# Performance work log

Measured on AMD Instinct MI355X. Metric: run time of the kernel, lower is better.

The kernel has to match this reference:

```python
import jax, jax.numpy as jnp
import numpy as np
import math

ANCHORS = np.array([[[10,13],[16,30],[33,23]],
                    [[30,61],[62,45],[59,119]],
                    [[116,90],[156,198],[373,326]]], dtype=np.float32)
STRIDES = [8.0, 16.0, 32.0]
BALANCE = [4.0, 1.0, 0.4]
LAMBDA_BOX, LAMBDA_OBJ, LAMBDA_CLS = 0.05, 1.0, 0.5
ANCHOR_T = 4.0
CP, CN = 1.0, 0.0  # label_smoothing = 0
EPS = 1e-7


def _bce(x, t):
    # BCEWithLogits, elementwise, numerically stable
    return jnp.maximum(x, 0.) - x * t + jnp.log1p(jnp.exp(-jnp.abs(x)))


def _ciou(b1, b2):
    # b1, b2: (M, 4) xyxy
    ix1 = jnp.maximum(b1[:, 0], b2[:, 0]); iy1 = jnp.maximum(b1[:, 1], b2[:, 1])
    ix2 = jnp.minimum(b1[:, 2], b2[:, 2]); iy2 = jnp.minimum(b1[:, 3], b2[:, 3])
    inter = jnp.clip(ix2 - ix1, 0.) * jnp.clip(iy2 - iy1, 0.)
    a1 = (b1[:, 2] - b1[:, 0]) * (b1[:, 3] - b1[:, 1])
    a2 = (b2[:, 2] - b2[:, 0]) * (b2[:, 3] - b2[:, 1])
    union = a1 + a2 - inter + EPS
    iou = inter / union
    ex1 = jnp.minimum(b1[:, 0], b2[:, 0]); ey1 = jnp.minimum(b1[:, 1], b2[:, 1])
    ex2 = jnp.maximum(b1[:, 2], b2[:, 2]); ey2 = jnp.maximum(b1[:, 3], b2[:, 3])
    c2 = (ex2 - ex1) ** 2 + (ey2 - ey1) ** 2 + EPS
    # center distance^2: centers are (x1+x2)/2
    rho2 = ((b1[:, 0] + b1[:, 2] - b2[:, 0] - b2[:, 2]) ** 2 +
            (b1[:, 1] + b1[:, 3] - b2[:, 1] - b2[:, 3]) ** 2) / 4.
    w1 = b1[:, 2] - b1[:, 0]; h1 = b1[:, 3] - b1[:, 1]
    w2 = b2[:, 2] - b2[:, 0]; h2 = b2[:, 3] - b2[:, 1]
    v = (4. / math.pi ** 2) * (jnp.arctan(w2 / (h2 + EPS)) - jnp.arctan(w1 / (h1 + EPS))) ** 2
    alpha = jax.lax.stop_gradient(v / (1. - iou + v + EPS))  # torch.no_grad()
    return iou - rho2 / c2 - alpha * v


def _layer_loss(pred, targets, anchor, balance):
    # pred: (B, na, H, W, 5+nc); targets: (nt, 6); anchor: (na, 2) in grid units
    B, na, H, W, C = pred.shape
    nc = C - 5
    nt = targets.shape[0]
    gain = jnp.array([1., 1., W, H, W, H], jnp.float32)
    t = targets * gain  # (nt, 6): [b, cls, gx, gy, gw, gh]
    # anchor-ratio filter
    r = t[:, 4:6][None] / (anchor[:, None] + 1e-16)            # (na, nt, 2)
    anchor_ok = jnp.max(jnp.maximum(r, 1. / r), axis=2) < ANCHOR_T  # (na, nt)
    # neighbor-cell selection masks (center + 4 neighbors)
    gxy = t[:, 2:4]
    gxi = jnp.floor(gxy)
    frac = gxy - gxi
    jm = (frac[:, 0] > .5) & (gxi[:, 0] < W - 1)
    km = (frac[:, 1] > .5) & (gxi[:, 1] < H - 1)
    lm = (frac[:, 0] < .5) & (gxi[:, 0] > 0)
    mm = (frac[:, 1] < .5) & (gxi[:, 1] > 0)
    sel = jnp.stack([jnp.ones_like(jm), jm, km, lm, mm])       # (5, nt)
    valid = sel[:, None, :] & anchor_ok[None]                  # (5, na, nt)
    off = jnp.array([[0, 0], [1, 0], [0, 1], [-1, 0], [0, -1]], jnp.float32)
    gxy_e = gxy[None] - off[:, None]                           # (5, nt, 2)
    gi = jnp.clip(jnp.floor(gxy_e).astype(jnp.int32), 0,
                  jnp.array([W - 1, H - 1], jnp.int32))        # (5, nt, 2)
    txy = gxy_e - gi.astype(jnp.float32)                       # offset-form xy
    gwh = t[:, 4:6]
    tbox = jnp.concatenate([txy - gwh[None] / 2., txy + gwh[None] / 2.], -1)  # (5, nt, 4)
    # flatten fixed-size candidate set (5 * na * nt), masked by `valid`
    shp = (5, na, nt)
    b_idx = jnp.broadcast_to(t[:, 0].astype(jnp.int32)[None, None], shp).reshape(-1)
    cls_i = jnp.broadcast_to(t[:, 1].astype(jnp.int32)[None, None], shp).reshape(-1)
    a_idx = jnp.broadcast_to(jnp.arange(na)[None, :, None], shp).reshape(-1)
    gx = jnp.broadcast_to(gi[:, None, :, 0], shp).reshape(-1)
    gy = jnp.broadcast_to(gi[:, None, :, 1], shp).reshape(-1)
    tbox_f = jnp.broadcast_to(tbox[:, None], shp + (4,)).reshape(-1, 4)
    vmask = valid.reshape(-1).astype(pred.dtype)
    cnt = vmask.sum()
    # fancy-indexed gather of matched predictions
    pm = pred[b_idx, a_idx, gy, gx]                            # (M, C)
    pxy = jax.nn.sigmoid(pm[:, :2]) * 2. - 0.5
    pwh = (jax.nn.sigmoid(pm[:, 2:4]) * 2.) ** 2 * anchor[a_idx]
    pbox = jnp.concatenate([pxy - pwh / 2., pxy + pwh / 2.], -1)
    ciou = _ciou(pbox, tbox_f)
    lbox = jnp.where(cnt > 0, jnp.sum((1. - ciou) * vmask) / jnp.maximum(cnt, 1.), 0.)
    # objectness target scatter (detached, clamped CIoU); invalid write 0 -> no-op under max
    tobj = jnp.zeros(pred.shape[:4], pred.dtype)
    vals = jax.lax.stop_gradient(jnp.clip(ciou, 0.) * vmask)
    tobj = tobj.at[b_idx, a_idx, gy, gx].max(vals)
    lobj = jnp.mean(_bce(pred[..., 4], tobj)) * balance
    # classification (mean over matched rows x nc elems)
    ct = CN + (CP - CN) * jax.nn.one_hot(cls_i, nc, dtype=pm.dtype)
    lcls = jnp.where(cnt > 0,
                     jnp.sum(_bce(pm[:, 5:], ct) * vmask[:, None]) / jnp.maximum(cnt * nc, 1.),
                     0.)
    return lbox, lobj, lcls


def _forward(pred0, pred1, pred2, targets):
    B = pred0.shape[0]
    preds = [pred0, pred1, pred2]
    lb = lo = lc = 0.
    for i in range(3):
        anchor = jnp.asarray(ANCHORS[i]) / STRIDES[i]
        bx, ob, cl = _layer_loss(preds[i], targets, anchor, BALANCE[i])
        lb = lb + bx; lo = lo + ob; lc = lc + cl
    return (LAMBDA_BOX * lb + LAMBDA_OBJ * lo + LAMBDA_CLS * lc) * B


def setup_inputs() -> dict:
    key = jax.random.key(0)
    ks = jax.random.split(key, 7)
    B, NT = 16, 300
    pred0 = jax.random.normal(ks[0], (B, 3, 80, 80, 85), jnp.float32)
    pred1 = jax.random.normal(ks[1], (B, 3, 40, 40, 85), jnp.float32)
    pred2 = jax.random.normal(ks[2], (B, 3, 20, 20, 85), jnp.float32)
    b = jax.random.randint(ks[3], (NT, 1), 0, B).astype(jnp.float32)
    c = jax.random.randint(ks[4], (NT, 1), 0, 80).astype(jnp.float32)
    cxy = jax.random.uniform(ks[5], (NT, 2), jnp.float32, 0.02, 0.98)
    wh = jax.random.uniform(ks[6], (NT, 2), jnp.float32, 0.02, 0.3)
    targets = jnp.concatenate([b, c, cxy, wh], axis=1)  # (NT, 6)
    return {"pred0": pred0, "pred1": pred1, "pred2": pred2, "targets": targets}


def reference(pred0, pred1, pred2, targets):
    return _forward(pred0, pred1, pred2, targets)
```

## Files before the change

kernel.cpp:

```cpp
#include <hip/hip_runtime.h>
#include <math.h>

#define EPSF 1e-7f
#define NT 256

__device__ __constant__ float d_anch[3][3][2] = {
    {{10.f/8.f,  13.f/8.f},  {16.f/8.f,  30.f/8.f},  {33.f/8.f,  23.f/8.f}},
    {{30.f/16.f, 61.f/16.f}, {62.f/16.f, 45.f/16.f}, {59.f/16.f, 119.f/16.f}},
    {{116.f/32.f,90.f/32.f}, {156.f/32.f,198.f/32.f},{373.f/32.f,326.f/32.f}},
};

__device__ __forceinline__ float bce0(float x) {
    return fmaxf(x, 0.0f) + log1pf(expf(-fabsf(x)));
}
__device__ __forceinline__ float bcef(float x, float t) {
    return fmaxf(x, 0.0f) - x * t + log1pf(expf(-fabsf(x)));
}
__device__ __forceinline__ float sigm(float x) {
    return 1.0f / (1.0f + expf(-x));
}

__device__ __forceinline__ float wave_reduce(float v) {
    #pragma unroll
    for (int off = 32; off > 0; off >>= 1) v += __shfl_down(v, off, 64);
    return v;
}

__global__ void __launch_bounds__(NT)
stream_kernel(const float* __restrict__ pred0,
              const float* __restrict__ pred1,
              const float* __restrict__ pred2,
              float* __restrict__ tobj,
              float* __restrict__ objpart,
              int n0, int n1, int n2)
{
    int N = n0 + n1 + n2;
    int base = blockIdx.x * (NT * 4) + threadIdx.x;
    float acc = 0.0f;
    #pragma unroll
    for (int k = 0; k < 4; ++k) {
        int idx = base + k * NT;
        if (idx < N) {
            tobj[idx] = 0.0f;
            const float* pred; int cell; float w;
            if (idx < n0)           { pred = pred0; cell = idx;           w = 4.0f / (float)n0; }
            else if (idx < n0 + n1) { pred = pred1; cell = idx - n0;      w = 1.0f / (float)n1; }
            else                    { pred = pred2; cell = idx - n0 - n1; w = 0.4f / (float)n2; }
            acc += w * bce0(pred[(size_t)cell * 85 + 4]);
        }
    }
    __shared__ float s[4];
    float r = wave_reduce(acc);
    if ((threadIdx.x & 63) == 0) s[threadIdx.x >> 6] = r;
    __syncthreads();
    if (threadIdx.x == 0)
        objpart[blockIdx.x] = s[0] + s[1] + s[2] + s[3];
}

__global__ void __launch_bounds__(NT)
entry_kernel(const float* __restrict__ pred0,
             const float* __restrict__ pred1,
             const float* __restrict__ pred2,
             const float* __restrict__ targets,
             int nt, int bpl,
             float* __restrict__ tobj_base,
             float* __restrict__ blockpart,
             int n0, int n1, int n2)
{
    int layer = blockIdx.x / bpl;
    int sub   = blockIdx.x % bpl;
    int wid   = threadIdx.x >> 6;
    int lane  = threadIdx.x & 63;
    int perLayer = 15 * nt;
    int eL = sub * 4 + wid;

    const float* pred; float* tobj; int H, W; float wl;
    if (layer == 0)      { pred = pred0; tobj = tobj_base;           H = 80; W = 80; wl = 4.0f / (float)n0; }
    else if (layer == 1) { pred = pred1; tobj = tobj_base + n0;      H = 40; W = 40; wl = 1.0f / (float)n1; }
    else                 { pred = pred2; tobj = tobj_base + n0 + n1; H = 20; W = 20; wl = 0.4f / (float)n2; }

    float lbox = 0.0f, cnt = 0.0f, corr = 0.0f, clsacc = 0.0f;

    if (eL < perLayer) {
        int t = eL % nt;
        int a = (eL / nt) % 3;
        int o = eL / (nt * 3);

        const float* tg = targets + t * 6;
        float tb = tg[0], tc = tg[1];
        float gx = tg[2] * (float)W, gy = tg[3] * (float)H;
        float gw = tg[4] * (float)W, gh = tg[5] * (float)H;

        float aw = d_anch[layer][a][0], ah = d_anch[layer][a][1];
        float rw = gw / (aw + 1e-16f), rh = gh / (ah + 1e-16f);
        float rmax = fmaxf(fmaxf(rw, 1.0f / rw), fmaxf(rh, 1.0f / rh));
        bool aok = rmax < 4.0f;

        float fxi = floorf(gx), fyi = floorf(gy);
        float fx = gx - fxi, fy = gy - fyi;
        bool selo;
        switch (o) {
            case 0: selo = true; break;
            case 1: selo = (fx > 0.5f) && (fxi < (float)(W - 1)); break;
            case 2: selo = (fy > 0.5f) && (fyi < (float)(H - 1)); break;
            case 3: selo = (fx < 0.5f) && (fxi > 0.0f); break;
            default: selo = (fy < 0.5f) && (fyi > 0.0f); break;
        }

        if (aok && selo) {
            float ox = (o == 1) ? 1.0f : (o == 3) ? -1.0f : 0.0f;
            float oy = (o == 2) ? 1.0f : (o == 4) ? -1.0f : 0.0f;
            float gex = gx - ox, gey = gy - oy;
            int gix = min(max((int)floorf(gex), 0), W - 1);
            int giy = min(max((int)floorf(gey), 0), H - 1);
            float txc = gex - (float)gix, tyc = gey - (float)giy;
            float tx1 = txc - gw * 0.5f, ty1 = tyc - gh * 0.5f;
            float tx2 = txc + gw * 0.5f, ty2 = tyc + gh * 0.5f;

            int b = (int)tb, cls = (int)tc;
            int cell = (int)(((((size_t)b * 3 + a) * H + giy) * W + gix));
            const float* pm = pred + (size_t)cell * 85;

            float p0 = pm[0], p1v = pm[1], p2v = pm[2], p3 = pm[3];
            float pxc = sigm(p0) * 2.0f - 0.5f;
            float pyc = sigm(p1v) * 2.0f - 0.5f;
            float sw = sigm(p2v) * 2.0f;
            float sh = sigm(p3) * 2.0f;
            float pw = sw * sw * aw, ph = sh * sh * ah;
            float px1 = pxc - pw * 0.5f, py1 = pyc - ph * 0.5f;
            float px2 = pxc + pw * 0.5f, py2 = pyc + ph * 0.5f;

            float ix1 = fmaxf(px1, tx1), iy1 = fmaxf(py1, ty1);
            float ix2 = fminf(px2, tx2), iy2 = fminf(py2, ty2);
            float inter = fmaxf(ix2 - ix1, 0.0f) * fmaxf(iy2 - iy1, 0.0f);
            float a1 = (px2 - px1) * (py2 - py1);
            float a2 = (tx2 - tx1) * (ty2 - ty1);
            float uni = a1 + a2 - inter + EPSF;
            float iou = inter / uni;
            float ex1 = fminf(px1, tx1), ey1 = fminf(py1, ty1);
            float ex2 = fmaxf(px2, tx2), ey2 = fmaxf(py2, ty2);
            float cw = ex2 - ex1, chh = ey2 - ey1;
            float c2 = cw * cw + chh * chh + EPSF;
            float dx = px1 + px2 - tx1 - tx2;
            float dy = py1 + py2 - ty1 - ty2;
            float rho2 = (dx * dx + dy * dy) * 0.25f;
            float w1 = px2 - px1, h1 = py2 - py1;
            float w2 = tx2 - tx1, h2 = ty2 - ty1;
            float dat = atanf(w2 / (h2 + EPSF)) - atanf(w1 / (h1 + EPSF));
            float v = 0.40528473f * dat * dat;
            float alpha = v / (1.0f - iou + v + EPSF);
            float ciou = iou - rho2 / c2 - alpha * v;

            if (lane == 0) {
                lbox = 1.0f - ciou;
                cnt = 1.0f;
                float vobj = fmaxf(ciou, 0.0f);
                unsigned int oldb = atomicMax((unsigned int*)&tobj[cell],
                                              __float_as_uint(vobj));
                float old = __uint_as_float(oldb);
                float nw = fmaxf(vobj, old);
                corr = wl * pm[4] * (nw - old);
            }

            float xc = pm[5 + lane];
            clsacc = bcef(xc, (lane == cls) ? 1.0f : 0.0f);
            if (lane < 16) {
                float xc2 = pm[69 + lane];
                clsacc += bcef(xc2, ((64 + lane) == cls) ? 1.0f : 0.0f);
            }
        }
    }

    float rb = wave_reduce(lbox);
    float rc = wave_reduce(cnt);
    float rl = wave_reduce(clsacc);
    float rr = wave_reduce(corr);
    __shared__ float s[4][4];
    if (lane == 0) {
        s[wid][0] = rb; s[wid][1] = rc; s[wid][2] = rl; s[wid][3] = rr;
    }
    __syncthreads();
    if (threadIdx.x < 4) {
        float v = s[0][threadIdx.x] + s[1][threadIdx.x] +
                  s[2][threadIdx.x] + s[3][threadIdx.x];
        blockpart[(size_t)blockIdx.x * 4 + threadIdx.x] = v;
    }
}

__global__ void __launch_bounds__(NT)
final_kernel(const float* __restrict__ objpart, int nb1,
             const float* __restrict__ blockpart, int bpl,
             float* __restrict__ out, int B)
{
    __shared__ float s[4];
    __shared__ float comp[11];
    int tid = threadIdx.x;
    int lane = tid & 63;
    int wid = tid >> 6;

    float v = 0.0f;
    for (int i = tid; i < nb1; i += NT) v += objpart[i];
    v = wave_reduce(v);
    if (lane == 0) s[wid] = v;
    __syncthreads();
    if (tid == 0) comp[9] = s[0] + s[1] + s[2] + s[3];
    __syncthreads();

    for (int c = 0; c < 4; ++c) {
        for (int L = 0; L < 3; ++L) {
            float v2 = 0.0f;
            if (c < 3) {
                for (int i = tid; i < bpl; i += NT)
                    v2 += blockpart[(size_t)(L * bpl + i) * 4 + c];
            } else if (L == 0) {
                for (int i = tid; i < 3 * bpl; i += NT)
                    v2 += blockpart[(size_t)i * 4 + 3];
            } else continue;
            v2 = wave_reduce(v2);
            if (lane == 0) s[wid] = v2;
            __syncthreads();
            if (tid == 0) {
                float r = s[0] + s[1] + s[2] + s[3];
                if (c < 3) comp[L * 3 + c] = r; else comp[10] = r;
            }
            __syncthreads();
        }
    }

    if (tid == 0) {
        float lobj = comp[9] - comp[10];
        float lb = 0.0f, lc = 0.0f;
        for (int L = 0; L < 3; ++L) {
            float cb = comp[L * 3 + 0], cc = comp[L * 3 + 1], cl = comp[L * 3 + 2];
            if (cc > 0.0f) {
                lb += cb / fmaxf(cc, 1.0f);
                lc += cl / fmaxf(cc * 80.0f, 1.0f);
            }
        }
        out[0] = (0.05f * lb + lobj + 0.5f * lc) * (float)B;
    }
}

extern "C" void kernel_launch(void* const* d_in, const int* in_sizes, int n_in,
                              void* d_out, int out_size, void* d_ws, size_t ws_size,
                              hipStream_t stream) {
    const float* pred0 = (const float*)d_in[0];
    const float* pred1 = (const float*)d_in[1];
    const float* pred2 = (const float*)d_in[2];
    const float* targets = (const float*)d_in[3];

    int B = in_sizes[0] / (3 * 80 * 80 * 85);
    int nt = in_sizes[3] / 6;
    int n0 = B * 3 * 80 * 80;
    int n1 = B * 3 * 40 * 40;
    int n2 = B * 3 * 20 * 20;
    int N = n0 + n1 + n2;
    int NB1 = (N + NT * 4 - 1) / (NT * 4);
    int perLayer = 15 * nt;
    int bpl = (perLayer + 3) / 4;
    int grid2 = 3 * bpl;

    float* tobj = (float*)d_ws;
    float* objpart = tobj + N;
    float* blockpart = objpart + NB1;

    stream_kernel<<<NB1, NT, 0, stream>>>(
        pred0, pred1, pred2, tobj, objpart, n0, n1, n2);
    entry_kernel<<<grid2, NT, 0, stream>>>(
        pred0, pred1, pred2, targets, nt, bpl, tobj, blockpart, n0, n1, n2);
    final_kernel<<<1, NT, 0, stream>>>(
        objpart, NB1, blockpart, bpl, (float*)d_out, B);
}
```

Before: 41.41 us.

## Replace strided objectness gather with coalesced float4 sweep fused into target kernel

The objectness BCE pass no longer loads one float per 85-float cell. Instead a fixed set of blocks streams the whole prediction tensors as coalesced float4 loads and keeps only the lanes that hold channel 4. These sweep blocks are merged into the same launch as the per-target box/class kernel, and zeroing of tobj moves to its own small vectorized kernel. The aim is fully coalesced memory traffic and overlap of the two phases, at the cost of reading every byte of the predictions rather than only the cache lines that contain objectness values.

New measurement: 64.88 us. +56.7%, slower.

```diff
diff --git a/kernel.cpp b/kernel.cpp
--- a/kernel.cpp
+++ b/kernel.cpp
@@ -3,6 +3,8 @@
 
 #define EPSF 1e-7f
 #define NT 256
+#define SWEEP_BLOCKS 1536
+#define ZERO_BLOCKS 512
 
 __device__ __constant__ float d_anch[3][3][2] = {
     {{10.f/8.f,  13.f/8.f},  {16.f/8.f,  30.f/8.f},  {33.f/8.f,  23.f/8.f}},
@@ -19,7 +21,6 @@
 __device__ __forceinline__ float sigm(float x) {
     return 1.0f / (1.0f + expf(-x));
 }
-
 __device__ __forceinline__ float wave_reduce(float v) {
     #pragma unroll
     for (int off = 32; off > 0; off >>= 1) v += __shfl_down(v, off, 64);
@@ -27,57 +28,65 @@
 }
 
 __global__ void __launch_bounds__(NT)
-stream_kernel(const float* __restrict__ pred0,
-              const float* __restrict__ pred1,
-              const float* __restrict__ pred2,
-              float* __restrict__ tobj,
-              float* __restrict__ objpart,
-              int n0, int n1, int n2)
+zero_kernel(float4* __restrict__ p, int n4)
 {
-    int N = n0 + n1 + n2;
-    int base = blockIdx.x * (NT * 4) + threadIdx.x;
-    float acc = 0.0f;
-    #pragma unroll
-    for (int k = 0; k < 4; ++k) {
-        int idx = base + k * NT;
-        if (idx < N) {
-            tobj[idx] = 0.0f;
-            const float* pred; int cell; float w;
-            if (idx < n0)           { pred = pred0; cell = idx;           w = 4.0f / (float)n0; }
-            else if (idx < n0 + n1) { pred = pred1; cell = idx - n0;      w = 1.0f / (float)n1; }
-            else                    { pred = pred2; cell = idx - n0 - n1; w = 0.4f / (float)n2; }
-            acc += w * bce0(pred[(size_t)cell * 85 + 4]);
-        }
-    }
-    __shared__ float s[4];
-    float r = wave_reduce(acc);
-    if ((threadIdx.x & 63) == 0) s[threadIdx.x >> 6] = r;
-    __syncthreads();
-    if (threadIdx.x == 0)
-        objpart[blockIdx.x] = s[0] + s[1] + s[2] + s[3];
+    for (int i = blockIdx.x * NT + threadIdx.x; i < n4; i += ZERO_BLOCKS * NT)
+        p[i] = make_float4(0.f, 0.f, 0.f, 0.f);
 }
 
 __global__ void __launch_bounds__(NT)
-entry_kernel(const float* __restrict__ pred0,
-             const float* __restrict__ pred1,
-             const float* __restrict__ pred2,
-             const float* __restrict__ targets,
-             int nt, int bpl,
-             float* __restrict__ tobj_base,
-             float* __restrict__ blockpart,
-             int n0, int n1, int n2)
+work_kernel(const float* __restrict__ pred0,
+            const float* __restrict__ pred1,
+            const float* __restrict__ pred2,
+            const float* __restrict__ targets,
+            int nt, int bpl,
+            float* __restrict__ tobj_base,
+            float* __restrict__ objpart,
+            float* __restrict__ blockpart,
+            int n0, int n1, int n2)
 {
-    int layer = blockIdx.x / bpl;
-    int sub   = blockIdx.x % bpl;
+    float w0 = 4.0f / (float)n0, w1 = 1.0f / (float)n1, w2 = 0.4f / (float)n2;
+
+    if (blockIdx.x < SWEEP_BLOCKS) {
+        unsigned f40 = (unsigned)n0 / 4u * 85u;
+        unsigned f41 = (unsigned)n1 / 4u * 85u;
+        unsigned f42 = (unsigned)n2 / 4u * 85u;
+        unsigned totalF4 = f40 + f41 + f42;
+        float acc = 0.0f;
+        for (unsigned f = blockIdx.x * NT + threadIdx.x; f < totalF4;
+             f += SWEEP_BLOCKS * NT) {
+            const float4* src; unsigned l; float w;
+            if (f < f40)              { src = (const float4*)pred0; l = f;              w = w0; }
+            else if (f < f40 + f41)   { src = (const float4*)pred1; l = f - f40;        w = w1; }
+            else                      { src = (const float4*)pred2; l = f - f40 - f41;  w = w2; }
+            float4 q = src[l];
+            unsigned m = (4u * l) % 85u;
+            if (m >= 1u && m <= 4u) {
+                float v = (m == 4u) ? q.x : (m == 3u) ? q.y : (m == 2u) ? q.z : q.w;
+                acc += w * bce0(v);
+            }
+        }
+        __shared__ float s[4];
+        float r = wave_reduce(acc);
+        if ((threadIdx.x & 63) == 0) s[threadIdx.x >> 6] = r;
+        __syncthreads();
+        if (threadIdx.x == 0)
+            objpart[blockIdx.x] = s[0] + s[1] + s[2] + s[3];
+        return;
+    }
+
+    int eb    = blockIdx.x - SWEEP_BLOCKS;
+    int layer = eb / bpl;
+    int sub   = eb % bpl;
     int wid   = threadIdx.x >> 6;
     int lane  = threadIdx.x & 63;
     int perLayer = 15 * nt;
     int eL = sub * 4 + wid;
 
     const float* pred; float* tobj; int H, W; float wl;
-    if (layer == 0)      { pred = pred0; tobj = tobj_base;           H = 80; W = 80; wl = 4.0f / (float)n0; }
-    else if (layer == 1) { pred = pred1; tobj = tobj_base + n0;      H = 40; W = 40; wl = 1.0f / (float)n1; }
-    else                 { pred = pred2; tobj = tobj_base + n0 + n1; H = 20; W = 20; wl = 0.4f / (float)n2; }
+    if (layer == 0)      { pred = pred0; tobj = tobj_base;           H = 80; W = 80; wl = w0; }
+    else if (layer == 1) { pred = pred1; tobj = tobj_base + n0;      H = 40; W = 40; wl = w1; }
+    else                 { pred = pred2; tobj = tobj_base + n0 + n1; H = 20; W = 20; wl = w2; }
 
     float lbox = 0.0f, cnt = 0.0f, corr = 0.0f, clsacc = 0.0f;
 
@@ -144,9 +153,9 @@
             float dx = px1 + px2 - tx1 - tx2;
             float dy = py1 + py2 - ty1 - ty2;
             float rho2 = (dx * dx + dy * dy) * 0.25f;
-            float w1 = px2 - px1, h1 = py2 - py1;
-            float w2 = tx2 - tx1, h2 = ty2 - ty1;
-            float dat = atanf(w2 / (h2 + EPSF)) - atanf(w1 / (h1 + EPSF));
+            float w1f = px2 - px1, h1 = py2 - py1;
+            float w2f = tx2 - tx1, h2 = ty2 - ty1;
+            float dat = atanf(w2f / (h2 + EPSF)) - atanf(w1f / (h1 + EPSF));
             float v = 0.40528473f * dat * dat;
             float alpha = v / (1.0f - iou + v + EPSF);
             float ciou = iou - rho2 / c2 - alpha * v;
@@ -175,15 +184,15 @@
     float rc = wave_reduce(cnt);
     float rl = wave_reduce(clsacc);
     float rr = wave_reduce(corr);
-    __shared__ float s[4][4];
+    __shared__ float s2[4][4];
     if (lane == 0) {
-        s[wid][0] = rb; s[wid][1] = rc; s[wid][2] = rl; s[wid][3] = rr;
+        s2[wid][0] = rb; s2[wid][1] = rc; s2[wid][2] = rl; s2[wid][3] = rr;
     }
     __syncthreads();
     if (threadIdx.x < 4) {
-        float v = s[0][threadIdx.x] + s[1][threadIdx.x] +
-                  s[2][threadIdx.x] + s[3][threadIdx.x];
-        blockpart[(size_t)blockIdx.x * 4 + threadIdx.x] = v;
+        float v = s2[0][threadIdx.x] + s2[1][threadIdx.x] +
+                  s2[2][threadIdx.x] + s2[3][threadIdx.x];
+        blockpart[(size_t)eb * 4 + threadIdx.x] = v;
     }
 }
 
@@ -255,19 +264,18 @@
     int n1 = B * 3 * 40 * 40;
     int n2 = B * 3 * 20 * 20;
     int N = n0 + n1 + n2;
-    int NB1 = (N + NT * 4 - 1) / (NT * 4);
     int perLayer = 15 * nt;
     int bpl = (perLayer + 3) / 4;
-    int grid2 = 3 * bpl;
+    int grid2 = SWEEP_BLOCKS + 3 * bpl;
 
     float* tobj = (float*)d_ws;
     float* objpart = tobj + N;
-    float* blockpart = objpart + NB1;
-
-    stream_kernel<<<NB1, NT, 0, stream>>>(
-        pred0, pred1, pred2, tobj, objpart, n0, n1, n2);
-    entry_kernel<<<grid2, NT, 0, stream>>>(
-        pred0, pred1, pred2, targets, nt, bpl, tobj, blockpart, n0, n1, n2);
+    float* blockpart = objpart + SWEEP_BLOCKS;
+
+    zero_kernel<<<ZERO_BLOCKS, NT, 0, stream>>>((float4*)tobj, N / 4);
+    work_kernel<<<grid2, NT, 0, stream>>>(
+        pred0, pred1, pred2, targets, nt, bpl, tobj,
+        objpart, blockpart, n0, n1, n2);
     final_kernel<<<1, NT, 0, stream>>>(
-        objpart, NB1, blockpart, bpl, (float*)d_out, B);
-}
+        objpart, SWEEP_BLOCKS, blockpart, bpl, (float*)d_out, B);
+}
```

## Replace per-block partial arrays with padded global atomic accumulators

Applied to the files above, without the earlier changes.

Both the stream and entry kernels now atomically add their block-reduced sums into 11 padded global slots instead of writing per-block partials. The final kernel becomes a single-thread combine with no reduction loops. The stream kernel also processes 8 elements per thread instead of 4, halving its block count. In exchange there is an extra memset launch and atomic contention on shared slots, and float atomic ordering makes the summation order nondeterministic.

Result: slower. 70.42 us (+70.1%).

```diff
diff --git a/kernel.cpp b/kernel.cpp
--- a/kernel.cpp
+++ b/kernel.cpp
@@ -3,6 +3,8 @@
 
 #define EPSF 1e-7f
 #define NT 256
+#define PAD 32
+
 
 __device__ __constant__ float d_anch[3][3][2] = {
     {{10.f/8.f,  13.f/8.f},  {16.f/8.f,  30.f/8.f},  {33.f/8.f,  23.f/8.f}},
@@ -19,7 +21,6 @@
 __device__ __forceinline__ float sigm(float x) {
     return 1.0f / (1.0f + expf(-x));
 }
-
 __device__ __forceinline__ float wave_reduce(float v) {
     #pragma unroll
     for (int off = 32; off > 0; off >>= 1) v += __shfl_down(v, off, 64);
@@ -31,14 +32,14 @@
               const float* __restrict__ pred1,
               const float* __restrict__ pred2,
               float* __restrict__ tobj,
-              float* __restrict__ objpart,
+              float* __restrict__ acc,
               int n0, int n1, int n2)
 {
     int N = n0 + n1 + n2;
-    int base = blockIdx.x * (NT * 4) + threadIdx.x;
-    float acc = 0.0f;
+    int base = blockIdx.x * (NT * 8) + threadIdx.x;
+    float a0 = 0.0f;
     #pragma unroll
-    for (int k = 0; k < 4; ++k) {
+    for (int k = 0; k < 8; ++k) {
         int idx = base + k * NT;
         if (idx < N) {
             tobj[idx] = 0.0f;
@@ -46,15 +47,16 @@
             if (idx < n0)           { pred = pred0; cell = idx;           w = 4.0f / (float)n0; }
             else if (idx < n0 + n1) { pred = pred1; cell = idx - n0;      w = 1.0f / (float)n1; }
             else                    { pred = pred2; cell = idx - n0 - n1; w = 0.4f / (float)n2; }
-            acc += w * bce0(pred[(size_t)cell * 85 + 4]);
-        }
-    }
+            a0 += w * bce0(pred[(size_t)cell * 85 + 4]);
+        }
+    }
+
     __shared__ float s[4];
-    float r = wave_reduce(acc);
+    float r = wave_reduce(a0);
     if ((threadIdx.x & 63) == 0) s[threadIdx.x >> 6] = r;
     __syncthreads();
     if (threadIdx.x == 0)
-        objpart[blockIdx.x] = s[0] + s[1] + s[2] + s[3];
+        atomicAdd(&acc[10 * PAD], s[0] + s[1] + s[2] + s[3]);
 }
 
 __global__ void __launch_bounds__(NT)
@@ -64,7 +66,7 @@
              const float* __restrict__ targets,
              int nt, int bpl,
              float* __restrict__ tobj_base,
-             float* __restrict__ blockpart,
+             float* __restrict__ acc,
              int n0, int n1, int n2)
 {
     int layer = blockIdx.x / bpl;
@@ -175,63 +177,33 @@
     float rc = wave_reduce(cnt);
     float rl = wave_reduce(clsacc);
     float rr = wave_reduce(corr);
-    __shared__ float s[4][4];
+    __shared__ float s2[4][4];
     if (lane == 0) {
-        s[wid][0] = rb; s[wid][1] = rc; s[wid][2] = rl; s[wid][3] = rr;
+        s2[wid][0] = rb; s2[wid][1] = rc; s2[wid][2] = rl; s2[wid][3] = rr;
     }
     __syncthreads();
     if (threadIdx.x < 4) {
-        float v = s[0][threadIdx.x] + s[1][threadIdx.x] +
-                  s[2][threadIdx.x] + s[3][threadIdx.x];
-        blockpart[(size_t)blockIdx.x * 4 + threadIdx.x] = v;
-    }
-}
-
-__global__ void __launch_bounds__(NT)
-final_kernel(const float* __restrict__ objpart, int nb1,
-             const float* __restrict__ blockpart, int bpl,
-             float* __restrict__ out, int B)
+        float v = s2[0][threadIdx.x] + s2[1][threadIdx.x] +
+                  s2[2][threadIdx.x] + s2[3][threadIdx.x];
+        int slot = (threadIdx.x == 0) ? (0 + layer)
+                 : (threadIdx.x == 1) ? (3 + layer)
+                 : (threadIdx.x == 2) ? (6 + layer)
+                 : 9;
+        atomicAdd(&acc[slot * PAD], v);
+    }
+}
+
+__global__ void final_kernel(const float* __restrict__ acc,
+                             float* __restrict__ out, int B)
 {
-    __shared__ float s[4];
-    __shared__ float comp[11];
-    int tid = threadIdx.x;
-    int lane = tid & 63;
-    int wid = tid >> 6;
-
-    float v = 0.0f;
-    for (int i = tid; i < nb1; i += NT) v += objpart[i];
-    v = wave_reduce(v);
-    if (lane == 0) s[wid] = v;
-    __syncthreads();
-    if (tid == 0) comp[9] = s[0] + s[1] + s[2] + s[3];
-    __syncthreads();
-
-    for (int c = 0; c < 4; ++c) {
+    if (threadIdx.x == 0 && blockIdx.x == 0) {
+        float lobj = acc[10 * PAD] - acc[9 * PAD];
+        float lb = 0.0f, lc = 0.0f;
+        #pragma unroll
         for (int L = 0; L < 3; ++L) {
-            float v2 = 0.0f;
-            if (c < 3) {
-                for (int i = tid; i < bpl; i += NT)
-                    v2 += blockpart[(size_t)(L * bpl + i) * 4 + c];
-            } else if (L == 0) {
-                for (int i = tid; i < 3 * bpl; i += NT)
-                    v2 += blockpart[(size_t)i * 4 + 3];
-            } else continue;
-            v2 = wave_reduce(v2);
-            if (lane == 0) s[wid] = v2;
-            __syncthreads();
-            if (tid == 0) {
-                float r = s[0] + s[1] + s[2] + s[3];
-                if (c < 3) comp[L * 3 + c] = r; else comp[10] = r;
-            }
-            __syncthreads();
-        }
-    }
-
-    if (tid == 0) {
-        float lobj = comp[9] - comp[10];
-        float lb = 0.0f, lc = 0.0f;
-        for (int L = 0; L < 3; ++L) {
-            float cb = comp[L * 3 + 0], cc = comp[L * 3 + 1], cl = comp[L * 3 + 2];
+            float cb = acc[(0 + L) * PAD];
+            float cc = acc[(3 + L) * PAD];
+            float cl = acc[(6 + L) * PAD];
             if (cc > 0.0f) {
                 lb += cb / fmaxf(cc, 1.0f);
                 lc += cl / fmaxf(cc * 80.0f, 1.0f);
@@ -255,19 +227,19 @@
     int n1 = B * 3 * 40 * 40;
     int n2 = B * 3 * 20 * 20;
     int N = n0 + n1 + n2;
-    int NB1 = (N + NT * 4 - 1) / (NT * 4);
+    int NB1 = (N + NT * 8 - 1) / (NT * 8);
     int perLayer = 15 * nt;
     int bpl = (perLayer + 3) / 4;
     int grid2 = 3 * bpl;
 
     float* tobj = (float*)d_ws;
-    float* objpart = tobj + N;
-    float* blockpart = objpart + NB1;
+    float* acc = tobj + N;
+
+    hipMemsetAsync(acc, 0, (size_t)11 * PAD * sizeof(float), stream);
 
     stream_kernel<<<NB1, NT, 0, stream>>>(
-        pred0, pred1, pred2, tobj, objpart, n0, n1, n2);
+        pred0, pred1, pred2, tobj, acc, n0, n1, n2);
     entry_kernel<<<grid2, NT, 0, stream>>>(
-        pred0, pred1, pred2, targets, nt, bpl, tobj, blockpart, n0, n1, n2);
-    final_kernel<<<1, NT, 0, stream>>>(
-        objpart, NB1, blockpart, bpl, (float*)d_out, B);
-}
+        pred0, pred1, pred2, targets, nt, bpl, tobj, acc, n0, n1, n2);
+    final_kernel<<<1, 64, 0, stream>>>(acc, (float*)d_out, B);
+}
```
